# Kernel tuning notes

Hardware: AMD Instinct MI355X
Metric: run time of the kernel (lower is better)

The kernel has to match this reference:

```python
import jax, jax.numpy as jnp
import numpy as np

NUM_EXPERT = 32
IN_FEAT = 256
OUT_FEAT = 256
TOTAL_TOKENS = 524288
CAPACITY = 16896  # static per-expert pad, > max expected count


def setup_inputs() -> dict:
    key = jax.random.key(0)
    k_inp, k_w = jax.random.split(key)
    inp = jax.random.normal(k_inp, (TOTAL_TOKENS, IN_FEAT), dtype=jnp.float32)
    # weight initialized like nn.Linear (kaiming-uniform-ish); scale of randn is fine for a numeric baseline
    weight = jax.random.normal(k_w, (NUM_EXPERT, OUT_FEAT, IN_FEAT), dtype=jnp.float32) * (1.0 / np.sqrt(IN_FEAT))
    # variable-sized expert groups summing exactly to TOTAL_TOKENS (tokens assumed pre-sorted by expert)
    rng = np.random.default_rng(0)
    counts = rng.multinomial(TOTAL_TOKENS, np.ones(NUM_EXPERT) / NUM_EXPERT)
    assert counts.max() <= CAPACITY and counts.sum() == TOTAL_TOKENS
    fwd_expert_count = jnp.asarray(counts, dtype=jnp.int64)
    return {"inp": inp, "weight": weight, "fwd_expert_count": fwd_expert_count, "capacity": CAPACITY}


def reference(inp, weight, fwd_expert_count, capacity):
    # Grouped GEMM: for expert e, out[seg_e] = inp[seg_e] @ weight[e].T
    E = weight.shape[0]
    T = inp.shape[0]
    counts = fwd_expert_count.astype(jnp.int32)
    cum = jnp.cumsum(counts)                       # [E] inclusive prefix sums
    starts = cum - counts                          # [E] segment starts
    tok = jnp.arange(T, dtype=jnp.int32)
    eid = jnp.searchsorted(cum, tok, side='right') # [T] expert id per token
    pos = tok - starts[eid]                        # [T] slot within expert group
    # Scatter tokens into padded per-expert buffer [E, capacity, in]
    buf = jnp.zeros((E, capacity, inp.shape[1]), dtype=inp.dtype).at[eid, pos].set(inp)
    # Batched matmul against per-expert weights [E, out, in] -> [E, capacity, out]
    y = jnp.einsum('eci,eoi->eco', buf, weight)
    # Gather back to token order [T, out]
    return y[eid, pos]
```

## Files before the change

kernel.cpp:

```cpp
#include <hip/hip_runtime.h>
#include <cstdint>
#include <cstddef>

#define NEXPERT 32
#define KIN 256
#define NOUT 256
#define NTOK 524288
#define BM 64

typedef float f32x4 __attribute__((ext_vector_type(4)));
typedef __bf16 bf16x8 __attribute__((ext_vector_type(8)));
typedef unsigned short u16;
typedef u16 u16x8 __attribute__((ext_vector_type(8)));
typedef unsigned int u32;

union BF8 { u16x8 u; bf16x8 b; };

__device__ __forceinline__ u16 f2bf(float f) {
  unsigned u = __float_as_uint(f);
  return (u16)((u + 0x7FFFu + ((u >> 16) & 1u)) >> 16);
}

#define GLDS(gp, lp) __builtin_amdgcn_global_load_lds(                      \
    (const __attribute__((address_space(1))) u32*)(gp),                      \
    (__attribute__((address_space(3))) u32*)(u32)(uintptr_t)(lp), 16, 0, 0)

#define VMW(n) asm volatile("s_waitcnt vmcnt(" n ")" ::: "memory")
#define BAR()  do { __builtin_amdgcn_sched_barrier(0);                       \
                    __builtin_amdgcn_s_barrier();                            \
                    __builtin_amdgcn_sched_barrier(0); } while (0)

__global__ void pack_w_kernel(const float* __restrict__ w, u16* __restrict__ wb) {
  const int t    = blockIdx.x * 256 + threadIdx.x;
  const int lane = t & 63;
  const int n16  = (t >> 6) & 15;
  const int kc   = (t >> 10) & 7;
  const int e    = t >> 13;
  const float* src = w + (size_t)e * 65536 + (size_t)(n16 * 16 + (lane & 15)) * 256
                       + kc * 32 + (lane >> 4) * 8;
  const float4 a = *reinterpret_cast<const float4*>(src);
  const float4 b = *reinterpret_cast<const float4*>(src + 4);
  u16x8 h;
  h[0]=f2bf(a.x); h[1]=f2bf(a.y); h[2]=f2bf(a.z); h[3]=f2bf(a.w);
  h[4]=f2bf(b.x); h[5]=f2bf(b.y); h[6]=f2bf(b.z); h[7]=f2bf(b.w);
  *reinterpret_cast<u16x8*>(wb + (size_t)t * 8) = h;
}

template<bool WSBF>
__device__ __forceinline__ void loadBstep(const u16* wEL, const float* wF,
                                          int wv, int l15, int lg, int s,
                                          BF8 (&d)[2][4]) {
  if (WSBF) {
#pragma unroll
    for (int c = 0; c < 2; ++c)
#pragma unroll
      for (int n = 0; n < 4; ++n)
        d[c][n].u = *reinterpret_cast<const u16x8*>(
            wEL + (size_t)(((2 * s + c) * 16 + (wv << 2) + n)) * 512);
  } else {
#pragma unroll
    for (int c = 0; c < 2; ++c)
#pragma unroll
      for (int n = 0; n < 4; ++n) {
        const float4* p = reinterpret_cast<const float4*>(
            wF + (size_t)((wv << 6) + (n << 4) + l15) * KIN + (2 * s + c) * 32 + lg * 8);
        const float4 x = p[0], y = p[1];
        u16x8 h;
        h[0]=f2bf(x.x); h[1]=f2bf(x.y); h[2]=f2bf(x.z); h[3]=f2bf(x.w);
        h[4]=f2bf(y.x); h[5]=f2bf(y.y); h[6]=f2bf(y.z); h[7]=f2bf(y.w);
        d[c][n].u = h;
      }
  }
}

__device__ __forceinline__ void computeStep(const char* sAc, int buf, int l15, int lg,
                                            const BF8 (&bfr)[2][4], f32x4 (&acc)[4][4]) {
  const char* abase = sAc + buf * 16384 + l15 * 256;
#pragma unroll
  for (int c = 0; c < 2; ++c) {
    BF8 af[4];
#pragma unroll
    for (int m = 0; m < 4; ++m) {
      const int g0 = (c << 3) + (lg << 1);
      const f32x4 fa = *reinterpret_cast<const f32x4*>(abase + m * 4096 + (((g0    ) ^ l15) << 4));
      const f32x4 fb = *reinterpret_cast<const f32x4*>(abase + m * 4096 + (((g0 + 1) ^ l15) << 4));
      af[m].b[0]=(__bf16)fa[0]; af[m].b[1]=(__bf16)fa[1];
      af[m].b[2]=(__bf16)fa[2]; af[m].b[3]=(__bf16)fa[3];
      af[m].b[4]=(__bf16)fb[0]; af[m].b[5]=(__bf16)fb[1];
      af[m].b[6]=(__bf16)fb[2]; af[m].b[7]=(__bf16)fb[3];
    }
#pragma unroll
    for (int m = 0; m < 4; ++m)
#pragma unroll
      for (int n = 0; n < 4; ++n)
        acc[m][n] = __builtin_amdgcn_mfma_f32_16x16x32_bf16(
            af[m].b, bfr[c][n].b, acc[m][n], 0, 0, 0);
  }
}

template<bool WSBF>
__global__ __launch_bounds__(256)
void moe_gemm_kernel(const float* __restrict__ inp,
                     const float* w32,
                     const u16* __restrict__ wpk,
                     const int* __restrict__ counts,
                     float* __restrict__ out)
{
  __shared__ float sA[4 * 64 * 64];

  const int tid  = threadIdx.x;
  const int lane = tid & 63;
  const int wv   = tid >> 6;
  const int l15  = lane & 15;
  const int lg   = lane >> 4;

  const long long* c64 = reinterpret_cast<const long long*>(counts);
  const long long p0 = c64[0];
  const bool is64 = (p0 >= 0 && p0 < (1ll << 31));
  int c = 0;
  if (lane < 32) c = is64 ? (int)c64[lane] : counts[lane];
#pragma unroll
  for (int d = 1; d < 32; d <<= 1) {
    const int o = __shfl_up(c, d, 64);
    if (lane >= d) c += o;
  }
  const int cum = (lane < 32) ? c : 0x7fffffff;

  const int t0 = blockIdx.x * BM;
  const int t1 = t0 + BM;

  const float* gp[4];
#pragma unroll
  for (int i = 0; i < 4; ++i) {
    const int r = (wv << 4) + (i << 2) + (lane >> 4);
    const int g = (lane & 15) ^ (r & 15);
    gp[i] = inp + (size_t)(t0 + r) * KIN + g * 4;
  }
  char* const sAc   = reinterpret_cast<char*>(sA);
  char* const lbase = sAc + wv * 4096;

  int rb = t0;
  int e  = __popcll(__ballot(cum <= t0));

  while (rb < t1) {
    const int re = min(t1, __shfl(cum, e));
    if (re > rb) {
      const u16*   wEL = wpk + (size_t)e * 65536 + (lane << 3);
      const float* wF  = w32 + ((size_t)e << 16);

      f32x4 acc[4][4];
      const f32x4 zero = {0.f, 0.f, 0.f, 0.f};
#pragma unroll
      for (int m = 0; m < 4; ++m)
#pragma unroll
        for (int n = 0; n < 4; ++n) acc[m][n] = zero;

      BF8 breA[2][4], breB[2][4];

      loadBstep<WSBF>(wEL, wF, wv, l15, lg, 0, breA);
#pragma unroll
      for (int i = 0; i < 4; ++i) GLDS(gp[i] +   0, lbase +     0 + i * 1024);
#pragma unroll
      for (int i = 0; i < 4; ++i) GLDS(gp[i] +  64, lbase + 16384 + i * 1024);

      loadBstep<WSBF>(wEL, wF, wv, l15, lg, 1, breB);
#pragma unroll
      for (int i = 0; i < 4; ++i) GLDS(gp[i] + 128, lbase + 32768 + i * 1024);
      VMW("16"); BAR();
      computeStep(sAc, 0, l15, lg, breA, acc);

      loadBstep<WSBF>(wEL, wF, wv, l15, lg, 2, breA);
#pragma unroll
      for (int i = 0; i < 4; ++i) GLDS(gp[i] + 192, lbase + 49152 + i * 1024);
      VMW("16"); BAR();
      computeStep(sAc, 1, l15, lg, breB, acc);

      loadBstep<WSBF>(wEL, wF, wv, l15, lg, 3, breB);
      VMW("12"); BAR();
      computeStep(sAc, 2, l15, lg, breA, acc);

      VMW("0"); BAR();
      computeStep(sAc, 3, l15, lg, breB, acc);

      const bool full = (rb == t0) & (re == t1);
      if (full) {
#pragma unroll
        for (int m = 0; m < 4; ++m) {
          const int rbase = t0 + (m << 4) + (lg << 2);
#pragma unroll
          for (int n = 0; n < 4; ++n) {
            float* op = out + (size_t)rbase * NOUT + (wv << 6) + (n << 4) + l15;
#pragma unroll
            for (int j = 0; j < 4; ++j) op[(size_t)j * NOUT] = acc[m][n][j];
          }
        }
      } else {
#pragma unroll
        for (int m = 0; m < 4; ++m) {
          const int rbase = t0 + (m << 4) + (lg << 2);
#pragma unroll
          for (int n = 0; n < 4; ++n) {
            float* op = out + (size_t)rbase * NOUT + (wv << 6) + (n << 4) + l15;
#pragma unroll
            for (int j = 0; j < 4; ++j) {
              const int rg = rbase + j;
              if (rg >= rb && rg < re) op[(size_t)j * NOUT] = acc[m][n][j];
            }
          }
        }
      }
    }
    rb = re > rb ? re : rb;
    ++e;
  }
}

extern "C" void kernel_launch(void* const* d_in, const int* in_sizes, int n_in,
                              void* d_out, int out_size, void* d_ws, size_t ws_size,
                              hipStream_t stream) {
  const float* inp    = (const float*)d_in[0];
  const float* w      = (const float*)d_in[1];
  const int*   counts = (const int*)d_in[2];
  float*       out    = (float*)d_out;

  const size_t wbytes = (size_t)NEXPERT * NOUT * KIN * 2;
  const bool usews = (ws_size >= wbytes);

  if (usews) {
    u16* wpk = (u16*)d_ws;
    pack_w_kernel<<<1024, 256, 0, stream>>>(w, wpk);
    moe_gemm_kernel<true><<<NTOK / BM, 256, 0, stream>>>(inp, w, wpk, counts, out);
  } else {
    moe_gemm_kernel<false><<<NTOK / BM, 256, 0, stream>>>(inp, w, nullptr, counts, out);
  }
}
```

Baseline: 219.7 us.

## Make GEMM blocks persistent over 16 tiles with cross-tile A prefetch and cached weights

Each block now processes 16 consecutive 64-row tiles instead of one. It keeps the current expert's full bf16 weight fragment in registers and reloads it only when the expert changes. A loads are staged two k-steps ahead across tile boundaries, so the LDS pipeline no longer drains between tiles. Rows belonging to a second expert inside a tile are deferred to a slower redo path that reads A directly from global memory. MFMA sections get raised wave priority and launch bounds request 2 blocks/CU. The trade-off is heavy register pressure from holding 128 weight registers, and far fewer blocks (512), which may reduce occupancy and load balance.

Measured after the change: 242.4 us. +10.3%, slower.

```diff
diff --git a/kernel.cpp b/kernel.cpp
--- a/kernel.cpp
+++ b/kernel.cpp
@@ -7,6 +7,7 @@
 #define NOUT 256
 #define NTOK 524288
 #define BM 64
+#define TPB 16
 
 typedef float f32x4 __attribute__((ext_vector_type(4)));
 typedef __bf16 bf16x8 __attribute__((ext_vector_type(8)));
@@ -47,29 +48,35 @@
 }
 
 template<bool WSBF>
-__device__ __forceinline__ void loadBstep(const u16* wEL, const float* wF,
-                                          int wv, int l15, int lg, int s,
-                                          BF8 (&d)[2][4]) {
+__device__ __forceinline__ void loadBexp(const u16* __restrict__ wpk, const float* w32,
+                                         int e, int wv, int l15, int lg, int lane,
+                                         BF8 (&B)[4][2][4]) {
   if (WSBF) {
-#pragma unroll
-    for (int c = 0; c < 2; ++c)
-#pragma unroll
-      for (int n = 0; n < 4; ++n)
-        d[c][n].u = *reinterpret_cast<const u16x8*>(
-            wEL + (size_t)(((2 * s + c) * 16 + (wv << 2) + n)) * 512);
+    const u16* wEL = wpk + ((size_t)e << 16) + (lane << 3);
+#pragma unroll
+    for (int s = 0; s < 4; ++s)
+#pragma unroll
+      for (int c = 0; c < 2; ++c)
+#pragma unroll
+        for (int n = 0; n < 4; ++n)
+          B[s][c][n].u = *reinterpret_cast<const u16x8*>(
+              wEL + (size_t)((2 * s + c) * 16 + (wv << 2) + n) * 512);
   } else {
 #pragma unroll
-    for (int c = 0; c < 2; ++c)
-#pragma unroll
-      for (int n = 0; n < 4; ++n) {
-        const float4* p = reinterpret_cast<const float4*>(
-            wF + (size_t)((wv << 6) + (n << 4) + l15) * KIN + (2 * s + c) * 32 + lg * 8);
-        const float4 x = p[0], y = p[1];
-        u16x8 h;
-        h[0]=f2bf(x.x); h[1]=f2bf(x.y); h[2]=f2bf(x.z); h[3]=f2bf(x.w);
-        h[4]=f2bf(y.x); h[5]=f2bf(y.y); h[6]=f2bf(y.z); h[7]=f2bf(y.w);
-        d[c][n].u = h;
-      }
+    for (int s = 0; s < 4; ++s)
+#pragma unroll
+      for (int c = 0; c < 2; ++c)
+#pragma unroll
+        for (int n = 0; n < 4; ++n) {
+          const float4* p = reinterpret_cast<const float4*>(
+              w32 + ((size_t)e << 16) +
+              (size_t)((wv << 6) + (n << 4) + l15) * KIN + (2 * s + c) * 32 + lg * 8);
+          const float4 x = p[0], y = p[1];
+          u16x8 h;
+          h[0]=f2bf(x.x); h[1]=f2bf(x.y); h[2]=f2bf(x.z); h[3]=f2bf(x.w);
+          h[4]=f2bf(y.x); h[5]=f2bf(y.y); h[6]=f2bf(y.z); h[7]=f2bf(y.w);
+          B[s][c][n].u = h;
+        }
   }
 }
 
@@ -89,17 +96,64 @@
       af[m].b[4]=(__bf16)fb[0]; af[m].b[5]=(__bf16)fb[1];
       af[m].b[6]=(__bf16)fb[2]; af[m].b[7]=(__bf16)fb[3];
     }
+    __builtin_amdgcn_s_setprio(1);
 #pragma unroll
     for (int m = 0; m < 4; ++m)
 #pragma unroll
       for (int n = 0; n < 4; ++n)
         acc[m][n] = __builtin_amdgcn_mfma_f32_16x16x32_bf16(
             af[m].b, bfr[c][n].b, acc[m][n], 0, 0, 0);
+    __builtin_amdgcn_s_setprio(0);
+  }
+}
+
+template<int DUMMY>
+__device__ void redoRun(const float* __restrict__ inp, int t0, int rb, int re,
+                        const BF8 (&B)[4][2][4], float* __restrict__ out,
+                        int wv, int l15, int lg) {
+  f32x4 acc[4][4];
+  const f32x4 zero = {0.f, 0.f, 0.f, 0.f};
+#pragma unroll
+  for (int m = 0; m < 4; ++m)
+#pragma unroll
+    for (int n = 0; n < 4; ++n) acc[m][n] = zero;
+#pragma unroll
+  for (int s = 0; s < 4; ++s)
+#pragma unroll
+    for (int c = 0; c < 2; ++c) {
+      BF8 af[4];
+#pragma unroll
+      for (int m = 0; m < 4; ++m) {
+        const float* p = inp + (size_t)(t0 + m * 16 + l15) * KIN + (2 * s + c) * 32 + lg * 8;
+        const float4 x = *reinterpret_cast<const float4*>(p);
+        const float4 y = *reinterpret_cast<const float4*>(p + 4);
+        af[m].u[0]=f2bf(x.x); af[m].u[1]=f2bf(x.y); af[m].u[2]=f2bf(x.z); af[m].u[3]=f2bf(x.w);
+        af[m].u[4]=f2bf(y.x); af[m].u[5]=f2bf(y.y); af[m].u[6]=f2bf(y.z); af[m].u[7]=f2bf(y.w);
+      }
+#pragma unroll
+      for (int m = 0; m < 4; ++m)
+#pragma unroll
+        for (int n = 0; n < 4; ++n)
+          acc[m][n] = __builtin_amdgcn_mfma_f32_16x16x32_bf16(
+              af[m].b, B[s][c][n].b, acc[m][n], 0, 0, 0);
+    }
+#pragma unroll
+  for (int m = 0; m < 4; ++m) {
+    const int rbase = t0 + (m << 4) + (lg << 2);
+#pragma unroll
+    for (int n = 0; n < 4; ++n) {
+      float* op = out + (size_t)rbase * NOUT + (wv << 6) + (n << 4) + l15;
+#pragma unroll
+      for (int j = 0; j < 4; ++j) {
+        const int rg = rbase + j;
+        if (rg >= rb && rg < re) op[(size_t)j * NOUT] = acc[m][n][j];
+      }
+    }
   }
 }
 
 template<bool WSBF>
-__global__ __launch_bounds__(256)
+__global__ __launch_bounds__(256, 2)
 void moe_gemm_kernel(const float* __restrict__ inp,
                      const float* w32,
                      const u16* __restrict__ wpk,
@@ -125,93 +179,102 @@
     if (lane >= d) c += o;
   }
   const int cum = (lane < 32) ? c : 0x7fffffff;
-
-  const int t0 = blockIdx.x * BM;
-  const int t1 = t0 + BM;
+  auto cumAt    = [&](int i) { return __shfl(cum, i, 64); };
+  auto expertOf = [&](int x) { return (int)__popcll(__ballot(cum <= x)); };
+
+  const int blk0 = blockIdx.x * (BM * TPB);
 
   const float* gp[4];
 #pragma unroll
   for (int i = 0; i < 4; ++i) {
     const int r = (wv << 4) + (i << 2) + (lane >> 4);
     const int g = (lane & 15) ^ (r & 15);
-    gp[i] = inp + (size_t)(t0 + r) * KIN + g * 4;
+    gp[i] = inp + (size_t)(blk0 + r) * KIN + g * 4;
   }
   char* const sAc   = reinterpret_cast<char*>(sA);
   char* const lbase = sAc + wv * 4096;
 
-  int rb = t0;
-  int e  = __popcll(__ballot(cum <= t0));
-
-  while (rb < t1) {
-    const int re = min(t1, __shfl(cum, e));
-    if (re > rb) {
-      const u16*   wEL = wpk + (size_t)e * 65536 + (lane << 3);
-      const float* wF  = w32 + ((size_t)e << 16);
-
-      f32x4 acc[4][4];
-      const f32x4 zero = {0.f, 0.f, 0.f, 0.f};
-#pragma unroll
-      for (int m = 0; m < 4; ++m)
-#pragma unroll
-        for (int n = 0; n < 4; ++n) acc[m][n] = zero;
-
-      BF8 breA[2][4], breB[2][4];
-
-      loadBstep<WSBF>(wEL, wF, wv, l15, lg, 0, breA);
-#pragma unroll
-      for (int i = 0; i < 4; ++i) GLDS(gp[i] +   0, lbase +     0 + i * 1024);
-#pragma unroll
-      for (int i = 0; i < 4; ++i) GLDS(gp[i] +  64, lbase + 16384 + i * 1024);
-
-      loadBstep<WSBF>(wEL, wF, wv, l15, lg, 1, breB);
-#pragma unroll
-      for (int i = 0; i < 4; ++i) GLDS(gp[i] + 128, lbase + 32768 + i * 1024);
-      VMW("16"); BAR();
-      computeStep(sAc, 0, l15, lg, breA, acc);
-
-      loadBstep<WSBF>(wEL, wF, wv, l15, lg, 2, breA);
-#pragma unroll
-      for (int i = 0; i < 4; ++i) GLDS(gp[i] + 192, lbase + 49152 + i * 1024);
-      VMW("16"); BAR();
-      computeStep(sAc, 1, l15, lg, breB, acc);
-
-      loadBstep<WSBF>(wEL, wF, wv, l15, lg, 3, breB);
-      VMW("12"); BAR();
-      computeStep(sAc, 2, l15, lg, breA, acc);
-
-      VMW("0"); BAR();
-      computeStep(sAc, 3, l15, lg, breB, acc);
-
-      const bool full = (rb == t0) & (re == t1);
-      if (full) {
-#pragma unroll
-        for (int m = 0; m < 4; ++m) {
-          const int rbase = t0 + (m << 4) + (lg << 2);
-#pragma unroll
-          for (int n = 0; n < 4; ++n) {
-            float* op = out + (size_t)rbase * NOUT + (wv << 6) + (n << 4) + l15;
-#pragma unroll
-            for (int j = 0; j < 4; ++j) op[(size_t)j * NOUT] = acc[m][n][j];
-          }
+  auto STAGE = [&](int gs) {
+    const size_t off = ((size_t)(gs >> 2) << 14) + (size_t)((gs & 3) << 6);
+    char* lb = lbase + ((gs & 3) << 14);
+#pragma unroll
+    for (int i = 0; i < 4; ++i) GLDS(gp[i] + off, lb + i * 1024);
+  };
+
+  BF8 B[4][2][4];
+  int cur_e = -1;
+  unsigned redo = 0;
+
+  STAGE(0); STAGE(1);
+
+  for (int t = 0; t < TPB; ++t) {
+    const int t0 = blk0 + (t << 6);
+    const int e  = expertOf(t0);
+    const int re = min(t0 + 64, cumAt(e));
+    const bool echg = (e != cur_e);
+    if (echg) { loadBexp<WSBF>(wpk, w32, e, wv, l15, lg, lane, B); cur_e = e; }
+    if (re < t0 + 64) redo |= (1u << t);
+
+    f32x4 acc[4][4];
+    const f32x4 zero = {0.f, 0.f, 0.f, 0.f};
+#pragma unroll
+    for (int m = 0; m < 4; ++m)
+#pragma unroll
+      for (int n = 0; n < 4; ++n) acc[m][n] = zero;
+
+    const bool lastT = (t == TPB - 1);
+#pragma unroll
+    for (int s = 0; s < 4; ++s) {
+      const int gs = (t << 2) + s;
+      if (s < 2 || !lastT) STAGE(gs + 2);
+      if (s == 0)      { if (echg) VMW("4"); else VMW("8"); }
+      else if (s == 2) { if (lastT) VMW("4"); else VMW("8"); }
+      else if (s == 3) { if (lastT) VMW("0"); else VMW("8"); }
+      else             VMW("8");
+      BAR();
+      computeStep(sAc, s, l15, lg, B[s], acc);
+    }
+
+    if (re == t0 + 64) {
+#pragma unroll
+      for (int m = 0; m < 4; ++m) {
+        const int rbase = t0 + (m << 4) + (lg << 2);
+#pragma unroll
+        for (int n = 0; n < 4; ++n) {
+          float* op = out + (size_t)rbase * NOUT + (wv << 6) + (n << 4) + l15;
+#pragma unroll
+          for (int j = 0; j < 4; ++j) op[(size_t)j * NOUT] = acc[m][n][j];
         }
-      } else {
-#pragma unroll
-        for (int m = 0; m < 4; ++m) {
-          const int rbase = t0 + (m << 4) + (lg << 2);
-#pragma unroll
-          for (int n = 0; n < 4; ++n) {
-            float* op = out + (size_t)rbase * NOUT + (wv << 6) + (n << 4) + l15;
-#pragma unroll
-            for (int j = 0; j < 4; ++j) {
-              const int rg = rbase + j;
-              if (rg >= rb && rg < re) op[(size_t)j * NOUT] = acc[m][n][j];
-            }
-          }
+      }
+    } else {
+#pragma unroll
+      for (int m = 0; m < 4; ++m) {
+        const int rbase = t0 + (m << 4) + (lg << 2);
+#pragma unroll
+        for (int n = 0; n < 4; ++n) {
+          float* op = out + (size_t)rbase * NOUT + (wv << 6) + (n << 4) + l15;
+#pragma unroll
+          for (int j = 0; j < 4; ++j)
+            if (rbase + j < re) op[(size_t)j * NOUT] = acc[m][n][j];
         }
       }
     }
-    rb = re > rb ? re : rb;
-    ++e;
+  }
+
+  while (redo) {
+    const int t = __builtin_ctz(redo); redo &= redo - 1;
+    const int t0 = blk0 + (t << 6), t1 = t0 + 64;
+    int e  = expertOf(t0);
+    int rb = min(t1, cumAt(e));
+    while (rb < t1) {
+      ++e;
+      const int re2 = min(t1, cumAt(e));
+      if (re2 > rb) {
+        loadBexp<WSBF>(wpk, w32, e, wv, l15, lg, lane, B);
+        redoRun<0>(inp, t0, rb, re2, B, out, wv, l15, lg);
+      }
+      rb = re2 > rb ? re2 : rb;
+    }
   }
 }
 
@@ -229,8 +292,8 @@
   if (usews) {
     u16* wpk = (u16*)d_ws;
     pack_w_kernel<<<1024, 256, 0, stream>>>(w, wpk);
-    moe_gemm_kernel<true><<<NTOK / BM, 256, 0, stream>>>(inp, w, wpk, counts, out);
+    moe_gemm_kernel<true><<<NTOK / (BM * TPB), 256, 0, stream>>>(inp, w, wpk, counts, out);
   } else {
-    moe_gemm_kernel<false><<<NTOK / BM, 256, 0, stream>>>(inp, w, nullptr, counts, out);
-  }
-}
+    moe_gemm_kernel<false><<<NTOK / (BM * TPB), 256, 0, stream>>>(inp, w, nullptr, counts, out);
+  }
+}
```

## Give each wave its own 16-row tile with full N and drop block barriers

Applied to the files above, without the earlier changes.

Each wave now owns 16 token rows across all 256 output columns instead of sharing a 64-row tile split by columns. Its A rows are staged in a private LDS region, so the block-wide barriers disappear and waves proceed independently. Expert boundaries are resolved per wave. B fragments are streamed in half-K chunks with vmcnt-based pipelining. In exchange, each wave must load the whole expert weight (four times more B traffic per block), and the non-first segments run with a serialized waitcnt-0 path.

Result: slower. 312.6 us (+42.2%).

```diff
diff --git a/kernel.cpp b/kernel.cpp
--- a/kernel.cpp
+++ b/kernel.cpp
@@ -6,7 +6,6 @@
 #define KIN 256
 #define NOUT 256
 #define NTOK 524288
-#define BM 64
 
 typedef float f32x4 __attribute__((ext_vector_type(4)));
 typedef __bf16 bf16x8 __attribute__((ext_vector_type(8)));
@@ -21,14 +20,16 @@
   return (u16)((u + 0x7FFFu + ((u >> 16) & 1u)) >> 16);
 }
 
+__device__ __forceinline__ void cvt8(const float4& x, const float4& y, BF8& o) {
+  o.u[0]=f2bf(x.x); o.u[1]=f2bf(x.y); o.u[2]=f2bf(x.z); o.u[3]=f2bf(x.w);
+  o.u[4]=f2bf(y.x); o.u[5]=f2bf(y.y); o.u[6]=f2bf(y.z); o.u[7]=f2bf(y.w);
+}
+
 #define GLDS(gp, lp) __builtin_amdgcn_global_load_lds(                      \
     (const __attribute__((address_space(1))) u32*)(gp),                      \
     (__attribute__((address_space(3))) u32*)(u32)(uintptr_t)(lp), 16, 0, 0)
 
 #define VMW(n) asm volatile("s_waitcnt vmcnt(" n ")" ::: "memory")
-#define BAR()  do { __builtin_amdgcn_sched_barrier(0);                       \
-                    __builtin_amdgcn_s_barrier();                            \
-                    __builtin_amdgcn_sched_barrier(0); } while (0)
 
 __global__ void pack_w_kernel(const float* __restrict__ w, u16* __restrict__ wb) {
   const int t    = blockIdx.x * 256 + threadIdx.x;
@@ -47,56 +48,36 @@
 }
 
 template<bool WSBF>
-__device__ __forceinline__ void loadBstep(const u16* wEL, const float* wF,
-                                          int wv, int l15, int lg, int s,
-                                          BF8 (&d)[2][4]) {
+__device__ __forceinline__ void loadBq(const u16* wEL, const float* wF,
+                                       int l15, int lg, int kc, int nb, BF8 (&d)[8]) {
   if (WSBF) {
 #pragma unroll
-    for (int c = 0; c < 2; ++c)
-#pragma unroll
-      for (int n = 0; n < 4; ++n)
-        d[c][n].u = *reinterpret_cast<const u16x8*>(
-            wEL + (size_t)(((2 * s + c) * 16 + (wv << 2) + n)) * 512);
+    for (int j = 0; j < 8; ++j)
+      d[j].u = *reinterpret_cast<const u16x8*>(wEL + (size_t)(kc * 16 + nb + j) * 512);
   } else {
 #pragma unroll
-    for (int c = 0; c < 2; ++c)
-#pragma unroll
-      for (int n = 0; n < 4; ++n) {
-        const float4* p = reinterpret_cast<const float4*>(
-            wF + (size_t)((wv << 6) + (n << 4) + l15) * KIN + (2 * s + c) * 32 + lg * 8);
-        const float4 x = p[0], y = p[1];
-        u16x8 h;
-        h[0]=f2bf(x.x); h[1]=f2bf(x.y); h[2]=f2bf(x.z); h[3]=f2bf(x.w);
-        h[4]=f2bf(y.x); h[5]=f2bf(y.y); h[6]=f2bf(y.z); h[7]=f2bf(y.w);
-        d[c][n].u = h;
-      }
-  }
-}
-
-__device__ __forceinline__ void computeStep(const char* sAc, int buf, int l15, int lg,
-                                            const BF8 (&bfr)[2][4], f32x4 (&acc)[4][4]) {
-  const char* abase = sAc + buf * 16384 + l15 * 256;
-#pragma unroll
-  for (int c = 0; c < 2; ++c) {
-    BF8 af[4];
-#pragma unroll
-    for (int m = 0; m < 4; ++m) {
-      const int g0 = (c << 3) + (lg << 1);
-      const f32x4 fa = *reinterpret_cast<const f32x4*>(abase + m * 4096 + (((g0    ) ^ l15) << 4));
-      const f32x4 fb = *reinterpret_cast<const f32x4*>(abase + m * 4096 + (((g0 + 1) ^ l15) << 4));
-      af[m].b[0]=(__bf16)fa[0]; af[m].b[1]=(__bf16)fa[1];
-      af[m].b[2]=(__bf16)fa[2]; af[m].b[3]=(__bf16)fa[3];
-      af[m].b[4]=(__bf16)fb[0]; af[m].b[5]=(__bf16)fb[1];
-      af[m].b[6]=(__bf16)fb[2]; af[m].b[7]=(__bf16)fb[3];
+    for (int j = 0; j < 8; ++j) {
+      const float4* p = reinterpret_cast<const float4*>(
+          wF + (size_t)((nb + j) * 16 + l15) * KIN + kc * 32 + lg * 8);
+      cvt8(p[0], p[1], d[j]);
     }
-#pragma unroll
-    for (int m = 0; m < 4; ++m)
-#pragma unroll
-      for (int n = 0; n < 4; ++n)
-        acc[m][n] = __builtin_amdgcn_mfma_f32_16x16x32_bf16(
-            af[m].b, bfr[c][n].b, acc[m][n], 0, 0, 0);
-  }
-}
+  }
+}
+
+__device__ __forceinline__ void loadAf(const char* abase, int c, int l15, int lg, BF8& af) {
+  const int g0 = (c << 3) + (lg << 1);
+  const f32x4 fa = *reinterpret_cast<const f32x4*>(abase + (((g0    ) ^ l15) << 4));
+  const f32x4 fb = *reinterpret_cast<const f32x4*>(abase + (((g0 + 1) ^ l15) << 4));
+  af.b[0]=(__bf16)fa[0]; af.b[1]=(__bf16)fa[1];
+  af.b[2]=(__bf16)fa[2]; af.b[3]=(__bf16)fa[3];
+  af.b[4]=(__bf16)fb[0]; af.b[5]=(__bf16)fb[1];
+  af.b[6]=(__bf16)fb[2]; af.b[7]=(__bf16)fb[3];
+}
+
+#define MFMA8(AF, BQ, NB)                                                    \
+  _Pragma("unroll") for (int j_ = 0; j_ < 8; ++j_)                           \
+    acc[(NB) + j_] = __builtin_amdgcn_mfma_f32_16x16x32_bf16(                \
+        (AF).b, (BQ)[j_].b, acc[(NB) + j_], 0, 0, 0);
 
 template<bool WSBF>
 __global__ __launch_bounds__(256)
@@ -106,7 +87,7 @@
                      const int* __restrict__ counts,
                      float* __restrict__ out)
 {
-  __shared__ float sA[4 * 64 * 64];
+  __shared__ float sA[16384];
 
   const int tid  = threadIdx.x;
   const int lane = tid & 63;
@@ -126,86 +107,111 @@
   }
   const int cum = (lane < 32) ? c : 0x7fffffff;
 
-  const int t0 = blockIdx.x * BM;
-  const int t1 = t0 + BM;
+  const int t0w = blockIdx.x * 64 + (wv << 4);
+  const int t1w = t0w + 16;
 
   const float* gp[4];
 #pragma unroll
   for (int i = 0; i < 4; ++i) {
-    const int r = (wv << 4) + (i << 2) + (lane >> 4);
-    const int g = (lane & 15) ^ (r & 15);
-    gp[i] = inp + (size_t)(t0 + r) * KIN + g * 4;
-  }
-  char* const sAc   = reinterpret_cast<char*>(sA);
-  char* const lbase = sAc + wv * 4096;
-
-  int rb = t0;
-  int e  = __popcll(__ballot(cum <= t0));
-
-  while (rb < t1) {
-    const int re = min(t1, __shfl(cum, e));
+    const int r = (i << 2) + (lane >> 4);
+    const int g = (lane & 15) ^ r;
+    gp[i] = inp + (size_t)(t0w + r) * KIN + g * 4;
+  }
+  char* const lbase = reinterpret_cast<char*>(sA) + wv * 16384;
+  const char* const rbase0 = lbase + l15 * 256;
+
+  int rb = t0w;
+  int e  = __popcll(__ballot(cum <= t0w));
+  bool first = true;
+
+  while (rb < t1w) {
+    const int re = min(t1w, __shfl(cum, e));
     if (re > rb) {
-      const u16*   wEL = wpk + (size_t)e * 65536 + (lane << 3);
+      const u16*   wEL = wpk + ((size_t)e << 16) + (lane << 3);
       const float* wF  = w32 + ((size_t)e << 16);
 
-      f32x4 acc[4][4];
+      f32x4 acc[16];
       const f32x4 zero = {0.f, 0.f, 0.f, 0.f};
 #pragma unroll
-      for (int m = 0; m < 4; ++m)
-#pragma unroll
-        for (int n = 0; n < 4; ++n) acc[m][n] = zero;
-
-      BF8 breA[2][4], breB[2][4];
-
-      loadBstep<WSBF>(wEL, wF, wv, l15, lg, 0, breA);
-#pragma unroll
-      for (int i = 0; i < 4; ++i) GLDS(gp[i] +   0, lbase +     0 + i * 1024);
-#pragma unroll
-      for (int i = 0; i < 4; ++i) GLDS(gp[i] +  64, lbase + 16384 + i * 1024);
-
-      loadBstep<WSBF>(wEL, wF, wv, l15, lg, 1, breB);
-#pragma unroll
-      for (int i = 0; i < 4; ++i) GLDS(gp[i] + 128, lbase + 32768 + i * 1024);
-      VMW("16"); BAR();
-      computeStep(sAc, 0, l15, lg, breA, acc);
-
-      loadBstep<WSBF>(wEL, wF, wv, l15, lg, 2, breA);
-#pragma unroll
-      for (int i = 0; i < 4; ++i) GLDS(gp[i] + 192, lbase + 49152 + i * 1024);
-      VMW("16"); BAR();
-      computeStep(sAc, 1, l15, lg, breB, acc);
-
-      loadBstep<WSBF>(wEL, wF, wv, l15, lg, 3, breB);
-      VMW("12"); BAR();
-      computeStep(sAc, 2, l15, lg, breA, acc);
-
-      VMW("0"); BAR();
-      computeStep(sAc, 3, l15, lg, breB, acc);
-
-      const bool full = (rb == t0) & (re == t1);
+      for (int n = 0; n < 16; ++n) acc[n] = zero;
+
+      BF8 b0[8], b1[8], af0, af1;
+
+      if (first) {
+#pragma unroll
+        for (int i = 0; i < 4; ++i) GLDS(gp[i] +   0, lbase +     0 + i * 1024);
+        loadBq<WSBF>(wEL, wF, l15, lg, 0, 0, b0);
+#pragma unroll
+        for (int i = 0; i < 4; ++i) GLDS(gp[i] +  64, lbase +  4096 + i * 1024);
+#pragma unroll
+        for (int i = 0; i < 4; ++i) GLDS(gp[i] + 128, lbase +  8192 + i * 1024);
+
+        loadBq<WSBF>(wEL, wF, l15, lg, 0, 8, b1);  VMW("16");
+        loadAf(rbase0 +     0, 0, l15, lg, af0);   MFMA8(af0, b0, 0);
+        loadBq<WSBF>(wEL, wF, l15, lg, 1, 0, b0);  VMW("8");
+        MFMA8(af0, b1, 8);
+        loadBq<WSBF>(wEL, wF, l15, lg, 1, 8, b1);  VMW("8");
+        loadAf(rbase0 +     0, 1, l15, lg, af1);   MFMA8(af1, b0, 0);
+        loadBq<WSBF>(wEL, wF, l15, lg, 2, 0, b0);
+#pragma unroll
+        for (int i = 0; i < 4; ++i) GLDS(gp[i] + 192, lbase + 12288 + i * 1024);
+        VMW("12");                                  MFMA8(af1, b1, 8);
+        loadBq<WSBF>(wEL, wF, l15, lg, 2, 8, b1);  VMW("12");
+        loadAf(rbase0 +  4096, 0, l15, lg, af0);   MFMA8(af0, b0, 0);
+        loadBq<WSBF>(wEL, wF, l15, lg, 3, 0, b0);  VMW("8");
+        MFMA8(af0, b1, 8);
+        loadBq<WSBF>(wEL, wF, l15, lg, 3, 8, b1);  VMW("8");
+        loadAf(rbase0 +  4096, 1, l15, lg, af1);   MFMA8(af1, b0, 0);
+        loadBq<WSBF>(wEL, wF, l15, lg, 4, 0, b0);  VMW("8");
+        MFMA8(af1, b1, 8);
+        loadBq<WSBF>(wEL, wF, l15, lg, 4, 8, b1);  VMW("8");
+        loadAf(rbase0 +  8192, 0, l15, lg, af0);   MFMA8(af0, b0, 0);
+        loadBq<WSBF>(wEL, wF, l15, lg, 5, 0, b0);  VMW("8");
+        MFMA8(af0, b1, 8);
+        loadBq<WSBF>(wEL, wF, l15, lg, 5, 8, b1);  VMW("8");
+        loadAf(rbase0 +  8192, 1, l15, lg, af1);   MFMA8(af1, b0, 0);
+        loadBq<WSBF>(wEL, wF, l15, lg, 6, 0, b0);  VMW("8");
+        MFMA8(af1, b1, 8);
+        loadBq<WSBF>(wEL, wF, l15, lg, 6, 8, b1);  VMW("8");
+        loadAf(rbase0 + 12288, 0, l15, lg, af0);   MFMA8(af0, b0, 0);
+        loadBq<WSBF>(wEL, wF, l15, lg, 7, 0, b0);  VMW("8");
+        MFMA8(af0, b1, 8);
+        loadBq<WSBF>(wEL, wF, l15, lg, 7, 8, b1);  VMW("8");
+        loadAf(rbase0 + 12288, 1, l15, lg, af1);   MFMA8(af1, b0, 0);
+        VMW("0");                                   MFMA8(af1, b1, 8);
+        first = false;
+      } else {
+#pragma unroll
+        for (int s = 0; s < 4; ++s) {
+          loadBq<WSBF>(wEL, wF, l15, lg, 2 * s, 0, b0);
+          loadBq<WSBF>(wEL, wF, l15, lg, 2 * s, 8, b1);
+          VMW("0");
+          loadAf(rbase0 + s * 4096, 0, l15, lg, af0);
+          MFMA8(af0, b0, 0); MFMA8(af0, b1, 8);
+          loadBq<WSBF>(wEL, wF, l15, lg, 2 * s + 1, 0, b0);
+          loadBq<WSBF>(wEL, wF, l15, lg, 2 * s + 1, 8, b1);
+          VMW("0");
+          loadAf(rbase0 + s * 4096, 1, l15, lg, af1);
+          MFMA8(af1, b0, 0); MFMA8(af1, b1, 8);
+        }
+      }
+
+      const bool full = (rb == t0w) & (re == t1w);
       if (full) {
 #pragma unroll
-        for (int m = 0; m < 4; ++m) {
-          const int rbase = t0 + (m << 4) + (lg << 2);
-#pragma unroll
-          for (int n = 0; n < 4; ++n) {
-            float* op = out + (size_t)rbase * NOUT + (wv << 6) + (n << 4) + l15;
-#pragma unroll
-            for (int j = 0; j < 4; ++j) op[(size_t)j * NOUT] = acc[m][n][j];
-          }
+        for (int n = 0; n < 16; ++n) {
+          float* op = out + (size_t)(t0w + (lg << 2)) * NOUT + n * 16 + l15;
+#pragma unroll
+          for (int j = 0; j < 4; ++j) op[(size_t)j * NOUT] = acc[n][j];
         }
       } else {
 #pragma unroll
-        for (int m = 0; m < 4; ++m) {
-          const int rbase = t0 + (m << 4) + (lg << 2);
-#pragma unroll
-          for (int n = 0; n < 4; ++n) {
-            float* op = out + (size_t)rbase * NOUT + (wv << 6) + (n << 4) + l15;
-#pragma unroll
-            for (int j = 0; j < 4; ++j) {
-              const int rg = rbase + j;
-              if (rg >= rb && rg < re) op[(size_t)j * NOUT] = acc[m][n][j];
-            }
+        for (int n = 0; n < 16; ++n) {
+          float* op = out + (size_t)(t0w + (lg << 2)) * NOUT + n * 16 + l15;
+#pragma unroll
+          for (int j = 0; j < 4; ++j) {
+            const int rg = t0w + (lg << 2) + j;
+            if (rg >= rb && rg < re) op[(size_t)j * NOUT] = acc[n][j];
           }
         }
       }
@@ -229,8 +235,8 @@
   if (usews) {
     u16* wpk = (u16*)d_ws;
     pack_w_kernel<<<1024, 256, 0, stream>>>(w, wpk);
-    moe_gemm_kernel<true><<<NTOK / BM, 256, 0, stream>>>(inp, w, wpk, counts, out);
+    moe_gemm_kernel<true><<<NTOK / 64, 256, 0, stream>>>(inp, w, wpk, counts, out);
   } else {
-    moe_gemm_kernel<false><<<NTOK / BM, 256, 0, stream>>>(inp, w, nullptr, counts, out);
-  }
-}
+    moe_gemm_kernel<false><<<NTOK / 64, 256, 0, stream>>>(inp, w, nullptr, counts, out);
+  }
+}
```
